# Kernel optimization log

Hardware: AMD Instinct MI355X
Metric: run time of the kernel (lower is better)

The kernel has to match this reference:

```python
import jax, jax.numpy as jnp
import numpy as np

B, S, D, HID, M = 2, 2048, 512, 1024, 64   # batch, seq, d_model, mlp hidden, meta tokens
K = 4                                       # depthwise causal conv kernel size
NH, DH = 8, 64                              # attention heads, head dim (NH*DH == D)
WIN = 256                                   # sliding attention window
L = 2                                       # n_hidden_layers in ResLinear
EPS = 1e-12                                 # F.normalize eps


def setup_inputs() -> dict:
    key = jax.random.key(0)
    ks = jax.random.split(key, 16)
    def g(k, shape, scale):
        return jax.random.normal(k, shape, dtype=jnp.float32) * scale
    s_d = 1.0 / np.sqrt(D).astype(np.float32)
    s_h = 1.0 / np.sqrt(HID).astype(np.float32)
    return {
        "x": jax.random.normal(ks[0], (B, S, D), dtype=jnp.float32),
        "meta_memory": g(ks[1], (M, D), s_d),
        # query LinearProjection: Linear(D->D) + depthwise causal Conv1d(K)
        "qp_w": g(ks[2], (D, D), s_d), "qp_b": jnp.zeros((D,), jnp.float32),
        "qp_conv": g(ks[3], (K, D), 1.0 / np.sqrt(K).astype(np.float32)),
        # ResLinear memory module
        "mlp_w_in": g(ks[4], (D, HID), s_d), "mlp_b_in": jnp.zeros((HID,), jnp.float32),
        "mlp_w_hid": g(ks[5], (L, HID, HID), s_h), "mlp_b_hid": jnp.zeros((L, HID), jnp.float32),
        "mlp_w_out": g(ks[6], (HID, D), s_h), "mlp_b_out": jnp.zeros((D,), jnp.float32),
        # sliding-window attention projections
        "swa_wq": g(ks[7], (D, D), s_d), "swa_bq": jnp.zeros((D,), jnp.float32),
        "swa_wk": g(ks[8], (D, D), s_d), "swa_bk": jnp.zeros((D,), jnp.float32),
        "swa_wv": g(ks[9], (D, D), s_d), "swa_bv": jnp.zeros((D,), jnp.float32),
        "swa_wo": g(ks[10], (D, D), s_d), "swa_bo": jnp.zeros((D,), jnp.float32),
    }


def _causal_depthwise_conv(x, kern):
    # x: [B,T,D], kern: [K,D]; out[t] = sum_k x[t-K+1+k] * kern[k]
    xp = jnp.pad(x, ((0, 0), (K - 1, 0), (0, 0)))
    T = x.shape[1]
    out = jnp.zeros_like(x)
    for k in range(K):  # small fixed K
        out = out + xp[:, k:k + T, :] * kern[k]
    return out


def _l2_norm(x):
    n = jnp.linalg.norm(x, axis=-1, keepdims=True)
    return x / jnp.maximum(n, EPS)


def reference(x, meta_memory, qp_w, qp_b, qp_conv,
              mlp_w_in, mlp_b_in, mlp_w_hid, mlp_b_hid, mlp_w_out, mlp_b_out,
              swa_wq, swa_bq, swa_wk, swa_bk, swa_wv, swa_bv, swa_wo, swa_bo):
    b = x.shape[0]
    # inject meta memory: [B, M+S, D]
    mm = jnp.broadcast_to(meta_memory[None], (b, M, D))
    xm = jnp.concatenate([mm, x], axis=1)
    T = xm.shape[1]
    # query projection (linear + causal depthwise conv) + l2 norm
    q = xm @ qp_w + qp_b
    q = _causal_depthwise_conv(q, qp_conv)
    q = _l2_norm(q)
    # ResLinear memory retrieval
    h = jax.nn.silu(q @ mlp_w_in + mlp_b_in)
    for i in range(L):
        h = h + jax.nn.silu(h @ mlp_w_hid[i] + mlp_b_hid[i])
    r = jax.nn.silu(h @ mlp_w_out + mlp_b_out)  # [B,T,D]
    qh = (r @ swa_wq + swa_bq).reshape(b, T, NH, DH)
    kh = (r @ swa_wk + swa_bk).reshape(b, T, NH, DH)
    vh = (r @ swa_wv + swa_bv).reshape(b, T, NH, DH)
    scores = jnp.einsum("bqhd,bkhd->bhqk", qh, kh) / np.float32(np.sqrt(DH))
    idx = jnp.arange(T)
    mask = (idx[:, None] >= idx[None, :]) & (idx[:, None] - idx[None, :] < WIN)
    scores = jnp.where(mask[None, None], scores, jnp.float32(-1e9))
    attn = jax.nn.softmax(scores, axis=-1)
    o = jnp.einsum("bhqk,bkhd->bqhd", attn, vh).reshape(b, T, D)
    o = o @ swa_wo + swa_bo
    return o[:, M:, :]  # drop meta tokens -> [B,S,D]
```

## Files before the change

kernel.cpp:

```cpp
#include <hip/hip_runtime.h>
#include <math.h>
#include <stdint.h>

#define BB 2
#define SS 2048
#define DD 512
#define HH 1024
#define MMETA 64
#define KCONV 4
#define NHH 8
#define DHH 64
#define WINN 256
#define TT (MMETA + SS)
#define BT (BB * TT)
#define QKV_N 1536

typedef __attribute__((ext_vector_type(8))) short short8v;
typedef __attribute__((ext_vector_type(4))) float f32x4;

__device__ __forceinline__ unsigned short f2bf(float f) {
    union { float f; unsigned u; } c; c.f = f;
    unsigned u = c.u;
    unsigned r = (u + 0x7fffu + ((u >> 16) & 1u)) >> 16;
    return (unsigned short)r;
}
__device__ __forceinline__ float bf2f(unsigned short h) {
    union { unsigned u; float f; } c; c.u = ((unsigned)h) << 16;
    return c.f;
}

__device__ __forceinline__ void gload_lds16(const void* g, void* l) {
    __builtin_amdgcn_global_load_lds(
        (const __attribute__((address_space(1))) unsigned int*)g,
        (__attribute__((address_space(3))) unsigned int*)l, 16, 0, 0);
}

template<int N>
__device__ __forceinline__ void vm_wait() {
    if constexpr (N == 0)      asm volatile("s_waitcnt vmcnt(0)" ::: "memory");
    else if constexpr (N == 2) asm volatile("s_waitcnt vmcnt(2)" ::: "memory");
    else if constexpr (N == 3) asm volatile("s_waitcnt vmcnt(3)" ::: "memory");
    else static_assert(N == 0, "unsupported vmcnt");
}

struct WJobs {
    const float* W[9];
    unsigned short* Wh[9];
    int K[9];
    int N[9];
    int base[10];
};

__global__ __launch_bounds__(256) void prep_all_k(
    WJobs jb,
    const float* __restrict__ x, const float* __restrict__ meta,
    unsigned short* __restrict__ xh,
    const float* __restrict__ bq, const float* __restrict__ bk,
    const float* __restrict__ bv, float* __restrict__ bqkv)
{
    __shared__ float tile[64][65];
    const int bid = blockIdx.x;
    const int tid = threadIdx.x;

    if (bid < 1088) {
        int j = 0;
        while (bid >= jb.base[j + 1]) ++j;
        const int local = bid - jb.base[j];
        const int K = jb.K[j], N = jb.N[j];
        const int nx = N >> 6;
        const int k0 = (local / nx) * 64, n0 = (local % nx) * 64;
        const float* W = jb.W[j];
        unsigned short* Wh = jb.Wh[j];
        #pragma unroll
        for (int i = 0; i < 16; ++i) {
            int lin = i * 256 + tid;
            int kr = lin >> 6, nc = lin & 63;
            tile[kr][nc] = W[(size_t)(k0 + kr) * N + n0 + nc];
        }
        __syncthreads();
        #pragma unroll
        for (int i = 0; i < 16; ++i) {
            int lin = i * 256 + tid;
            int nr = lin >> 6, kc = lin & 63;
            Wh[(size_t)(n0 + nr) * K + k0 + kc] = f2bf(tile[kc][nr]);
        }
    } else if (bid < 3200) {
        int idx = (bid - 1088) * 256 + tid;
        int row = idx >> 7, c4 = idx & 127;
        int b = row >= TT;
        int t = row - b * TT;
        float4 v = (t < MMETA) ? ((const float4*)(meta + (size_t)t * DD))[c4]
                               : ((const float4*)(x + ((size_t)b * SS + (t - MMETA)) * DD))[c4];
        ushort4 h;
        h.x = f2bf(v.x); h.y = f2bf(v.y); h.z = f2bf(v.z); h.w = f2bf(v.w);
        ((ushort4*)xh)[idx] = h;
    } else {
        int i = (bid - 3200) * 256 + tid;
        if (i < QKV_N) {
            float v;
            if (i < 512) v = bq[i];
            else if (i < 1024) v = bk[i - 512];
            else v = bv[i - 1024];
            bqkv[i] = v;
        }
    }
}

template<int BN, int GN, int EPI, bool DROPMETA>
__global__ __launch_bounds__(256, 3) void gemm_mfma_k(
    const unsigned short* __restrict__ Ah,
    const unsigned short* __restrict__ Wh,
    const float* __restrict__ bias,
    const unsigned short* __restrict__ resh,
    float* __restrict__ outf, unsigned short* __restrict__ outh,
    unsigned short* __restrict__ outl,
    unsigned short* __restrict__ vth,
    int K, int N)
{
    constexpr int BM = 64;
    constexpr int MF = 2;
    constexpr int NF = BN / 32;
    constexpr int ABYTES = BM * 64;
    constexpr int BBYTES = BN * 64;
    constexpr int BUFB = ABYTES + BBYTES;
    constexpr int LOADS = 1 + BN / 64;
    __shared__ short8v smem_v[(2 * BUFB) / 16];
    char* smem = (char*)smem_v;

    constexpr int NWG = 66 * GN;
    const int orig = blockIdx.x;
    const int swz = (orig & 7) * (NWG >> 3) + (orig >> 3);
    const int row0 = (swz / GN) * BM;
    const int n0 = (swz % GN) * BN;

    const int tid = threadIdx.x;
    const int l = tid & 63, wid = tid >> 6;
    const int wm = wid >> 1, wn = wid & 1;
    const int lr = l & 15, lg = l >> 4;

    const char* Ahg0 = (const char*)Ah + (size_t)row0 * K * 2;
    const char* Whg  = (const char*)Wh + (size_t)n0 * K * 2;

    int a_off[MF], b_off[NF];
    #pragma unroll
    for (int mf = 0; mf < MF; ++mf) {
        int r = wm * 32 + mf * 16 + lr;
        a_off[mf] = r * 64 + ((lg * 16) ^ (((r >> 1) & 3) << 4));
    }
    #pragma unroll
    for (int nf = 0; nf < NF; ++nf) {
        int r = wn * (BN / 2) + nf * 16 + lr;
        b_off[nf] = r * 64 + ((lg * 16) ^ (((r >> 1) & 3) << 4));
    }

    f32x4 acc[MF][NF];
    #pragma unroll
    for (int mf = 0; mf < MF; ++mf)
        #pragma unroll
        for (int nf = 0; nf < NF; ++nf) acc[mf][nf] = (f32x4){0.f, 0.f, 0.f, 0.f};

    const int NT = K / 32;

    auto stage = [&](int buf, int t) {
        char* lb = smem + buf * BUFB;
        const size_t kb = (size_t)t * 64;
        {
            int off = tid * 16;
            int row = off >> 6;
            int sc = (off & 63) ^ (((row >> 1) & 3) << 4);
            size_t gb = (size_t)row * (K * 2) + kb + sc;
            gload_lds16(Ahg0 + gb, lb + off);
        }
        #pragma unroll
        for (int it = 0; it < BBYTES / 4096; ++it) {
            int off = (it * 256 + tid) * 16;
            int row = off >> 6;
            int sc = (off & 63) ^ (((row >> 1) & 3) << 4);
            size_t gb = (size_t)row * (K * 2) + kb + sc;
            gload_lds16(Whg + gb, lb + ABYTES + off);
        }
    };

    stage(0, 0);

    int cur = 0;
    for (int t = 0; t < NT; ++t) {
        if (t + 1 < NT) {
            stage(cur ^ 1, t + 1);
            vm_wait<LOADS>();
        } else {
            vm_wait<0>();
        }
        __builtin_amdgcn_s_barrier();
        __builtin_amdgcn_sched_barrier(0);

        char* lb = smem + cur * BUFB;
        short8v ah[MF], bh[NF];
        #pragma unroll
        for (int mf = 0; mf < MF; ++mf)
            ah[mf] = *(const short8v*)(lb + a_off[mf]);
        #pragma unroll
        for (int nf = 0; nf < NF; ++nf)
            bh[nf] = *(const short8v*)(lb + ABYTES + b_off[nf]);
        __builtin_amdgcn_s_setprio(1);
        #pragma unroll
        for (int mf = 0; mf < MF; ++mf)
            #pragma unroll
            for (int nf = 0; nf < NF; ++nf)
                acc[mf][nf] = __builtin_amdgcn_mfma_f32_16x16x32_bf16(ah[mf], bh[nf], acc[mf][nf], 0, 0, 0);
        __builtin_amdgcn_s_setprio(0);
        __builtin_amdgcn_s_barrier();
        cur ^= 1;
    }

    #pragma unroll
    for (int mf = 0; mf < MF; ++mf) {
        #pragma unroll
        for (int nf = 0; nf < NF; ++nf) {
            int col = n0 + wn * (BN / 2) + nf * 16 + lr;
            float bv = bias[col];
            if (EPI == 4 && col >= 1024) {
                unsigned short hv[4];
                #pragma unroll
                for (int j = 0; j < 4; ++j)
                    hv[j] = f2bf(acc[mf][nf][j] + bv);
                int dg = col - 1024;
                size_t tok = (size_t)row0 + wm * 32 + mf * 16 + lg * 4;
                *(ushort4*)(vth + (size_t)dg * BT + tok) = *(ushort4*)hv;
            } else {
                #pragma unroll
                for (int j = 0; j < 4; ++j) {
                    int row = row0 + wm * 32 + mf * 16 + lg * 4 + j;
                    float v = acc[mf][nf][j] + bv;
                    if (EPI == 5 || EPI == 6) v = v / (1.f + __expf(-v));
                    size_t idx = (size_t)row * N + col;
                    if (EPI == 6) v += bf2f(resh[idx]);
                    if (EPI == 0) {
                        if (DROPMETA) {
                            int b = row >= TT;
                            int t2 = row - b * TT;
                            if (t2 >= MMETA)
                                outf[((size_t)b * SS + (t2 - MMETA)) * N + col] = v;
                        } else {
                            outf[idx] = v;
                        }
                    } else if (EPI == 5 || EPI == 6) {
                        outh[idx] = f2bf(v);
                    } else {
                        unsigned short hi = f2bf(v);
                        outh[idx] = hi;
                        outl[idx] = f2bf(v - bf2f(hi));
                    }
                }
            }
        }
    }
}

__global__ __launch_bounds__(256) void conv_norm8_k(
    const float* __restrict__ qlin, const float* __restrict__ convw,
    unsigned short* __restrict__ qh)
{
    __shared__ float qs[11][512];
    const int tid = threadIdx.x;
    const int r0 = blockIdx.x * 8;
    const int b = r0 >= TT;
    const int bstart = b * TT;

    const float4* ql4 = (const float4*)qlin;
    for (int i = tid; i < 11 * 128; i += 256) {
        int lrow = i >> 7, c4 = i & 127;
        int grow = r0 - 3 + lrow;
        float4 v = (grow >= bstart) ? ql4[(size_t)grow * 128 + c4]
                                    : (float4){0.f, 0.f, 0.f, 0.f};
        ((float4*)qs[lrow])[c4] = v;
    }
    __syncthreads();

    const int w = tid >> 6, lane = tid & 63;
    const int d0 = lane * 8;

    #pragma unroll
    for (int e = 0; e < 2; ++e) {
        const int lrow = w * 2 + e;
        const int rowg = r0 + lrow;
        float vals[8];
        #pragma unroll
        for (int j = 0; j < 8; ++j) vals[j] = 0.f;
        #pragma unroll
        for (int k = 0; k < KCONV; ++k) {
            const float* src = qs[lrow + k];
            const float* cw = convw + k * DD + d0;
            #pragma unroll
            for (int j = 0; j < 8; ++j)
                vals[j] += src[d0 + j] * cw[j];
        }
        float ss = 0.f;
        #pragma unroll
        for (int j = 0; j < 8; ++j) ss += vals[j] * vals[j];
        #pragma unroll
        for (int off = 32; off > 0; off >>= 1)
            ss += __shfl_xor(ss, off);
        float inv = 1.f / fmaxf(sqrtf(ss), 1e-12f);
        unsigned short hv[8];
        #pragma unroll
        for (int j = 0; j < 8; ++j)
            hv[j] = f2bf(vals[j] * inv);
        size_t base = (size_t)rowg * DD + d0;
        *(ushort4*)(qh + base) = *(ushort4*)hv;
        *(ushort4*)(qh + base + 4) = *(ushort4*)(hv + 4);
    }
}

__global__ __launch_bounds__(256, 2) void swa_flash_k(
    const unsigned short* __restrict__ qkvh, const unsigned short* __restrict__ qkvl,
    const unsigned short* __restrict__ vth,
    unsigned short* __restrict__ oh)
{
    __shared__ short8v lds_v[33792 / 16];
    char* lds = (char*)lds_v;
    char* Kh_lds = lds;
    char* Kl_lds = lds + 8192;
    char* Vh_lds = lds + 16384;
    char* P_lds  = lds + 24576;

    const int tid = threadIdx.x;
    const int lane = tid & 63, w = tid >> 6;
    const int l15 = lane & 15, lg = lane >> 4;
    const int q0 = blockIdx.x * 64;
    const int h = blockIdx.y, b = blockIdx.z;
    const int rowbase = b * TT;

    const int qrow = rowbase + q0 + w * 16 + l15;
    short8v qhf[2], qlf[2];
    #pragma unroll
    for (int kh = 0; kh < 2; ++kh) {
        size_t off = (size_t)qrow * QKV_N + h * 64 + kh * 32 + lg * 8;
        qhf[kh] = *(const short8v*)(qkvh + off);
        qlf[kh] = *(const short8v*)(qkvl + off);
    }

    f32x4 o_acc[4];
    #pragma unroll
    for (int td = 0; td < 4; ++td) o_acc[td] = (f32x4){0.f, 0.f, 0.f, 0.f};
    float m_r[4], l_r[4];
    #pragma unroll
    for (int r = 0; r < 4; ++r) { m_r[r] = -1e30f; l_r[r] = 0.f; }

    char* Pw = P_lds + w * 2304;

    for (int kt = 0; kt < 5; ++kt) {
        const int kst = q0 - 256 + kt * 64;
        if (kst + 64 <= 0) continue;
        __syncthreads();
        #pragma unroll
        for (int it = 0; it < 2; ++it) {
            int lin = it * 256 + tid;
            int r = lin >> 3, seg = lin & 7;
            int colb = (seg * 16) ^ ((r & 7) << 4);
            size_t gb = ((size_t)(rowbase + kst + r) * QKV_N + 512 + h * 64) * 2 + colb;
            gload_lds16((const char*)qkvh + gb, Kh_lds + lin * 16);
            gload_lds16((const char*)qkvl + gb, Kl_lds + lin * 16);
        }
        #pragma unroll
        for (int it = 0; it < 2; ++it) {
            int lin = it * 256 + tid;
            int dd = lin >> 3, seg = lin & 7;
            int colb = (seg * 16) ^ ((dd & 7) << 4);
            size_t gb = ((size_t)(h * 64 + dd) * BT + rowbase + kst) * 2 + colb;
            gload_lds16((const char*)vth + gb, Vh_lds + lin * 16);
        }
        __syncthreads();

        f32x4 s_fr[4];
        #pragma unroll
        for (int tj = 0; tj < 4; ++tj) s_fr[tj] = (f32x4){0.f, 0.f, 0.f, 0.f};
        #pragma unroll
        for (int tj = 0; tj < 4; ++tj) {
            int j = tj * 16 + l15;
            #pragma unroll
            for (int kh = 0; kh < 2; ++kh) {
                int colb = (kh * 64 + lg * 16) ^ ((j & 7) << 4);
                short8v kbh = *(const short8v*)(Kh_lds + j * 128 + colb);
                short8v kbl = *(const short8v*)(Kl_lds + j * 128 + colb);
                s_fr[tj] = __builtin_amdgcn_mfma_f32_16x16x32_bf16(qhf[kh], kbh, s_fr[tj], 0, 0, 0);
                s_fr[tj] = __builtin_amdgcn_mfma_f32_16x16x32_bf16(qhf[kh], kbl, s_fr[tj], 0, 0, 0);
                s_fr[tj] = __builtin_amdgcn_mfma_f32_16x16x32_bf16(qlf[kh], kbh, s_fr[tj], 0, 0, 0);
            }
        }
        #pragma unroll
        for (int tj = 0; tj < 4; ++tj) {
            int j = kst + tj * 16 + l15;
            #pragma unroll
            for (int r = 0; r < 4; ++r) {
                int i = q0 + w * 16 + lg * 4 + r;
                bool valid = (j <= i) && (i - j < WINN);
                s_fr[tj][r] = valid ? s_fr[tj][r] * 0.125f : -1e30f;
            }
        }
        float mx[4];
        #pragma unroll
        for (int r = 0; r < 4; ++r) {
            mx[r] = fmaxf(fmaxf(s_fr[0][r], s_fr[1][r]), fmaxf(s_fr[2][r], s_fr[3][r]));
            #pragma unroll
            for (int msk = 1; msk <= 8; msk <<= 1)
                mx[r] = fmaxf(mx[r], __shfl_xor(mx[r], msk));
            float mn = fmaxf(m_r[r], mx[r]);
            float sc = __expf(m_r[r] - mn);
            m_r[r] = mn;
            l_r[r] *= sc;
            #pragma unroll
            for (int td = 0; td < 4; ++td) o_acc[td][r] *= sc;
        }
        float rs[4] = {0.f, 0.f, 0.f, 0.f};
        #pragma unroll
        for (int tj = 0; tj < 4; ++tj) {
            #pragma unroll
            for (int r = 0; r < 4; ++r) {
                float p = __expf(s_fr[tj][r] - m_r[r]);
                rs[r] += p;
                ((unsigned short*)Pw)[(lg * 4 + r) * 72 + tj * 16 + l15] = f2bf(p);
            }
        }
        #pragma unroll
        for (int r = 0; r < 4; ++r) {
            #pragma unroll
            for (int msk = 1; msk <= 8; msk <<= 1)
                rs[r] += __shfl_xor(rs[r], msk);
            l_r[r] += rs[r];
        }
        short8v pa[2];
        #pragma unroll
        for (int jh = 0; jh < 2; ++jh)
            pa[jh] = *(const short8v*)(Pw + l15 * 144 + jh * 64 + lg * 16);
        #pragma unroll
        for (int td = 0; td < 4; ++td) {
            int drow = td * 16 + l15;
            #pragma unroll
            for (int jh = 0; jh < 2; ++jh) {
                int colb = (jh * 64 + lg * 16) ^ ((drow & 7) << 4);
                short8v vfh = *(const short8v*)(Vh_lds + drow * 128 + colb);
                o_acc[td] = __builtin_amdgcn_mfma_f32_16x16x32_bf16(pa[jh], vfh, o_acc[td], 0, 0, 0);
            }
        }
    }

    #pragma unroll
    for (int r = 0; r < 4; ++r) {
        float inv = 1.f / l_r[r];
        int row = rowbase + q0 + w * 16 + lg * 4 + r;
        #pragma unroll
        for (int td = 0; td < 4; ++td) {
            float v = o_acc[td][r] * inv;
            oh[(size_t)row * DD + h * 64 + td * 16 + l15] = f2bf(v);
        }
    }
}

extern "C" void kernel_launch(void* const* d_in, const int* in_sizes, int n_in,
                              void* d_out, int out_size, void* d_ws, size_t ws_size,
                              hipStream_t stream)
{
    const float* x       = (const float*)d_in[0];
    const float* meta    = (const float*)d_in[1];
    const float* qp_w    = (const float*)d_in[2];
    const float* qp_b    = (const float*)d_in[3];
    const float* qp_conv = (const float*)d_in[4];
    const float* w_in    = (const float*)d_in[5];
    const float* b_in    = (const float*)d_in[6];
    const float* w_hid   = (const float*)d_in[7];
    const float* b_hid   = (const float*)d_in[8];
    const float* w_out   = (const float*)d_in[9];
    const float* b_out   = (const float*)d_in[10];
    const float* wq      = (const float*)d_in[11];
    const float* bq      = (const float*)d_in[12];
    const float* wk      = (const float*)d_in[13];
    const float* bk      = (const float*)d_in[14];
    const float* wv      = (const float*)d_in[15];
    const float* bv      = (const float*)d_in[16];
    const float* wo      = (const float*)d_in[17];
    const float* bo      = (const float*)d_in[18];
    float* out = (float*)d_out;

    typedef unsigned short us;
    char* p = (char*)d_ws;
    auto alloc = [&](size_t n) { char* r = p; p += (n + 255) & ~(size_t)255; return r; };

    us* wqp_h   = (us*)alloc(512 * 512 * 2);
    us* win_h   = (us*)alloc(512 * 1024 * 2);
    us* whid0_h = (us*)alloc(1024 * 1024 * 2);
    us* whid1_h = (us*)alloc(1024 * 1024 * 2);
    us* wout_h  = (us*)alloc(1024 * 512 * 2);
    us* wqkv_h  = (us*)alloc((size_t)QKV_N * 512 * 2);
    us* wo_h    = (us*)alloc(512 * 512 * 2);
    float* bqkv = (float*)alloc(QKV_N * 4);

    const size_t H512 = (size_t)BT * 512 * 2;
    const size_t H1024 = (size_t)BT * 1024 * 2;
    char* RA = alloc(H512);
    char* RB = alloc((size_t)BT * 512 * 4);
    char* RC = alloc(H512);
    char* RD1 = alloc(H1024);
    char* RD2 = alloc(H1024);
    char* RF = alloc(2 * (size_t)BT * QKV_N * 2);
    char* RE = alloc(H512);

    us* xm = (us*)RA;
    float* qlin = (float*)RB;
    us* qn = (us*)RC;
    us* ha = (us*)RD1;
    us* hb = (us*)RD2;
    us* hc = (us*)RD1;
    us* r  = qn;
    us* qkv_h = (us*)RF;  us* qkv_l = (us*)(RF + (size_t)BT * QKV_N * 2);
    us* vt = (us*)RE;
    us* ob = (us*)RA;

    WJobs jb;
    const float* Ws[9]   = {qp_w, w_in, w_hid, w_hid + (size_t)1024 * 1024, w_out,
                            wq, wk, wv, wo};
    us* Whs[9] = {wqp_h, win_h, whid0_h, whid1_h, wout_h,
                  wqkv_h, wqkv_h + 512 * 512, wqkv_h + 2 * 512 * 512, wo_h};
    int Ks[9] = {512, 512, 1024, 1024, 1024, 512, 512, 512, 512};
    int Ns[9] = {512, 1024, 1024, 1024, 512, 512, 512, 512, 512};
    int acc_t = 0;
    for (int j = 0; j < 9; ++j) {
        jb.W[j] = Ws[j]; jb.Wh[j] = Whs[j];
        jb.K[j] = Ks[j]; jb.N[j] = Ns[j];
        jb.base[j] = acc_t;
        acc_t += (Ks[j] / 64) * (Ns[j] / 64);
    }
    jb.base[9] = acc_t;
    prep_all_k<<<3206, 256, 0, stream>>>(jb, x, meta, xm, bq, bk, bv, bqkv);

    gemm_mfma_k<64, 8, 0, false><<<528, 256, 0, stream>>>(
        xm, wqp_h, qp_b, nullptr, qlin, nullptr, nullptr, nullptr, 512, 512);
    conv_norm8_k<<<BT / 8, 256, 0, stream>>>(qlin, qp_conv, qn);
    gemm_mfma_k<128, 8, 5, false><<<528, 256, 0, stream>>>(
        qn, win_h, b_in, nullptr, nullptr, ha, nullptr, nullptr, 512, 1024);
    gemm_mfma_k<128, 8, 6, false><<<528, 256, 0, stream>>>(
        ha, whid0_h, b_hid, ha, nullptr, hb, nullptr, nullptr, 1024, 1024);
    gemm_mfma_k<128, 8, 6, false><<<528, 256, 0, stream>>>(
        hb, whid1_h, b_hid + HH, hb, nullptr, hc, nullptr, nullptr, 1024, 1024);
    gemm_mfma_k<64, 8, 5, false><<<528, 256, 0, stream>>>(
        hc, wout_h, b_out, nullptr, nullptr, r, nullptr, nullptr, 1024, 512);
    gemm_mfma_k<128, 12, 4, false><<<792, 256, 0, stream>>>(
        r, wqkv_h, bqkv, nullptr, nullptr, qkv_h, qkv_l, vt, 512, QKV_N);
    swa_flash_k<<<dim3(TT / 64, NHH, BB), 256, 0, stream>>>(qkv_h, qkv_l, vt, ob);
    gemm_mfma_k<64, 8, 0, true><<<528, 256, 0, stream>>>(
        ob, wo_h, bo, nullptr, out, nullptr, nullptr, nullptr, 512, 512);
}
```

Baseline: 144.4 us.

## Widen GEMM K-tile to 64 and double-buffer K/V loads in sliding-window attention

The GEMM kernel now stages 64-wide K slices per iteration instead of 32, with a new 128-byte-row XOR swizzle. This halves the number of barrier-separated iterations and doubles the MFMA work per sync, at the cost of more LDS per block. The attention kernel now double-buffers its K/V tiles in LDS, prefetching the next key block while computing the current one, and uses vmcnt-based waits instead of __syncthreads. The larger LDS footprint may reduce occupancy.

```diff
diff --git a/kernel.cpp b/kernel.cpp
--- a/kernel.cpp
+++ b/kernel.cpp
@@ -38,8 +38,8 @@
 template<int N>
 __device__ __forceinline__ void vm_wait() {
     if constexpr (N == 0)      asm volatile("s_waitcnt vmcnt(0)" ::: "memory");
-    else if constexpr (N == 2) asm volatile("s_waitcnt vmcnt(2)" ::: "memory");
-    else if constexpr (N == 3) asm volatile("s_waitcnt vmcnt(3)" ::: "memory");
+    else if constexpr (N == 4) asm volatile("s_waitcnt vmcnt(4)" ::: "memory");
+    else if constexpr (N == 6) asm volatile("s_waitcnt vmcnt(6)" ::: "memory");
     else static_assert(N == 0, "unsupported vmcnt");
 }
 
@@ -120,10 +120,10 @@
     constexpr int BM = 64;
     constexpr int MF = 2;
     constexpr int NF = BN / 32;
-    constexpr int ABYTES = BM * 64;
-    constexpr int BBYTES = BN * 64;
+    constexpr int ABYTES = BM * 128;
+    constexpr int BBYTES = BN * 128;
     constexpr int BUFB = ABYTES + BBYTES;
-    constexpr int LOADS = 1 + BN / 64;
+    constexpr int LOADS = BUFB / 4096;
     __shared__ short8v smem_v[(2 * BUFB) / 16];
     char* smem = (char*)smem_v;
 
@@ -141,16 +141,20 @@
     const char* Ahg0 = (const char*)Ah + (size_t)row0 * K * 2;
     const char* Whg  = (const char*)Wh + (size_t)n0 * K * 2;
 
-    int a_off[MF], b_off[NF];
+    int a_off[MF][2], b_off[NF][2];
     #pragma unroll
     for (int mf = 0; mf < MF; ++mf) {
         int r = wm * 32 + mf * 16 + lr;
-        a_off[mf] = r * 64 + ((lg * 16) ^ (((r >> 1) & 3) << 4));
+        #pragma unroll
+        for (int h = 0; h < 2; ++h)
+            a_off[mf][h] = r * 128 + ((h * 64 + lg * 16) ^ ((r & 7) << 4));
     }
     #pragma unroll
     for (int nf = 0; nf < NF; ++nf) {
         int r = wn * (BN / 2) + nf * 16 + lr;
-        b_off[nf] = r * 64 + ((lg * 16) ^ (((r >> 1) & 3) << 4));
+        #pragma unroll
+        for (int h = 0; h < 2; ++h)
+            b_off[nf][h] = r * 128 + ((h * 64 + lg * 16) ^ ((r & 7) << 4));
     }
 
     f32x4 acc[MF][NF];
@@ -159,23 +163,24 @@
         #pragma unroll
         for (int nf = 0; nf < NF; ++nf) acc[mf][nf] = (f32x4){0.f, 0.f, 0.f, 0.f};
 
-    const int NT = K / 32;
+    const int NT = K / 64;
 
     auto stage = [&](int buf, int t) {
         char* lb = smem + buf * BUFB;
-        const size_t kb = (size_t)t * 64;
-        {
-            int off = tid * 16;
-            int row = off >> 6;
-            int sc = (off & 63) ^ (((row >> 1) & 3) << 4);
+        const size_t kb = (size_t)t * 128;
+        #pragma unroll
+        for (int it = 0; it < ABYTES / 4096; ++it) {
+            int off = (it * 256 + tid) * 16;
+            int row = off >> 7;
+            int sc = (off & 127) ^ ((row & 7) << 4);
             size_t gb = (size_t)row * (K * 2) + kb + sc;
             gload_lds16(Ahg0 + gb, lb + off);
         }
         #pragma unroll
         for (int it = 0; it < BBYTES / 4096; ++it) {
             int off = (it * 256 + tid) * 16;
-            int row = off >> 6;
-            int sc = (off & 63) ^ (((row >> 1) & 3) << 4);
+            int row = off >> 7;
+            int sc = (off & 127) ^ ((row & 7) << 4);
             size_t gb = (size_t)row * (K * 2) + kb + sc;
             gload_lds16(Whg + gb, lb + ABYTES + off);
         }
@@ -195,19 +200,22 @@
         __builtin_amdgcn_sched_barrier(0);
 
         char* lb = smem + cur * BUFB;
-        short8v ah[MF], bh[NF];
-        #pragma unroll
-        for (int mf = 0; mf < MF; ++mf)
-            ah[mf] = *(const short8v*)(lb + a_off[mf]);
-        #pragma unroll
-        for (int nf = 0; nf < NF; ++nf)
-            bh[nf] = *(const short8v*)(lb + ABYTES + b_off[nf]);
         __builtin_amdgcn_s_setprio(1);
         #pragma unroll
-        for (int mf = 0; mf < MF; ++mf)
+        for (int h = 0; h < 2; ++h) {
+            short8v ah[MF], bh[NF];
+            #pragma unroll
+            for (int mf = 0; mf < MF; ++mf)
+                ah[mf] = *(const short8v*)(lb + a_off[mf][h]);
             #pragma unroll
             for (int nf = 0; nf < NF; ++nf)
-                acc[mf][nf] = __builtin_amdgcn_mfma_f32_16x16x32_bf16(ah[mf], bh[nf], acc[mf][nf], 0, 0, 0);
+                bh[nf] = *(const short8v*)(lb + ABYTES + b_off[nf][h]);
+            #pragma unroll
+            for (int mf = 0; mf < MF; ++mf)
+                #pragma unroll
+                for (int nf = 0; nf < NF; ++nf)
+                    acc[mf][nf] = __builtin_amdgcn_mfma_f32_16x16x32_bf16(ah[mf], bh[nf], acc[mf][nf], 0, 0, 0);
+        }
         __builtin_amdgcn_s_setprio(0);
         __builtin_amdgcn_s_barrier();
         cur ^= 1;
@@ -317,12 +325,9 @@
     const unsigned short* __restrict__ vth,
     unsigned short* __restrict__ oh)
 {
-    __shared__ short8v lds_v[33792 / 16];
+    __shared__ short8v lds_v[58368 / 16];
     char* lds = (char*)lds_v;
-    char* Kh_lds = lds;
-    char* Kl_lds = lds + 8192;
-    char* Vh_lds = lds + 16384;
-    char* P_lds  = lds + 24576;
+    char* P_lds = lds + 49152;
 
     const int tid = threadIdx.x;
     const int lane = tid & 63, w = tid >> 6;
@@ -349,18 +354,17 @@
 
     char* Pw = P_lds + w * 2304;
 
-    for (int kt = 0; kt < 5; ++kt) {
+    auto stage_kv = [&](int buf, int kt) {
+        char* base = lds + buf * 24576;
         const int kst = q0 - 256 + kt * 64;
-        if (kst + 64 <= 0) continue;
-        __syncthreads();
         #pragma unroll
         for (int it = 0; it < 2; ++it) {
             int lin = it * 256 + tid;
             int r = lin >> 3, seg = lin & 7;
             int colb = (seg * 16) ^ ((r & 7) << 4);
             size_t gb = ((size_t)(rowbase + kst + r) * QKV_N + 512 + h * 64) * 2 + colb;
-            gload_lds16((const char*)qkvh + gb, Kh_lds + lin * 16);
-            gload_lds16((const char*)qkvl + gb, Kl_lds + lin * 16);
+            gload_lds16((const char*)qkvh + gb, base + lin * 16);
+            gload_lds16((const char*)qkvl + gb, base + 8192 + lin * 16);
         }
         #pragma unroll
         for (int it = 0; it < 2; ++it) {
@@ -368,9 +372,28 @@
             int dd = lin >> 3, seg = lin & 7;
             int colb = (seg * 16) ^ ((dd & 7) << 4);
             size_t gb = ((size_t)(h * 64 + dd) * BT + rowbase + kst) * 2 + colb;
-            gload_lds16((const char*)vth + gb, Vh_lds + lin * 16);
-        }
-        __syncthreads();
+            gload_lds16((const char*)vth + gb, base + 16384 + lin * 16);
+        }
+    };
+
+    const int kt_min = (q0 >= 256) ? 0 : (256 - q0) / 64;
+    stage_kv(0, kt_min);
+
+    int bufi = 0;
+    for (int kt = kt_min; kt < 5; ++kt) {
+        const int kst = q0 - 256 + kt * 64;
+        if (kt + 1 < 5) {
+            stage_kv(bufi ^ 1, kt + 1);
+            vm_wait<6>();
+        } else {
+            vm_wait<0>();
+        }
+        __builtin_amdgcn_s_barrier();
+        __builtin_amdgcn_sched_barrier(0);
+
+        char* Kh_lds = lds + bufi * 24576;
+        char* Kl_lds = Kh_lds + 8192;
+        char* Vh_lds = Kh_lds + 16384;
 
         f32x4 s_fr[4];
         #pragma unroll
@@ -443,6 +466,8 @@
                 o_acc[td] = __builtin_amdgcn_mfma_f32_16x16x32_bf16(pa[jh], vfh, o_acc[td], 0, 0, 0);
             }
         }
+        __builtin_amdgcn_s_barrier();
+        bufi ^= 1;
     }
 
     #pragma unroll
```

After: 131.9 us (median of 2 runs). 8.6% less time.
